# Kernel optimization log

Hardware: AMD Instinct MI355X
Metric: run time of the kernel (lower is better)

The kernel has to match this reference:

```python
import jax, jax.numpy as jnp
import numpy as np

TAU = 2.0       # LIF membrane time constant (spikingjelly default)
ALPHA = 2.0     # ATan surrogate sharpness
EPS = 1e-5      # BN eps
NUM_HEADS = 12
PATCH = 2
LENTH = 256     # (H/PATCH)*(W/PATCH)

@jax.custom_vjp
def heaviside(x):
    return (x >= 0.0).astype(x.dtype)

def _hv_fwd(x):
    return heaviside(x), x

def _hv_bwd(x, g):
    sg = ALPHA / 2.0 / (1.0 + (jnp.pi / 2.0 * ALPHA * x) ** 2)  # ATan surrogate
    return (g * sg,)

heaviside.defvjp(_hv_fwd, _hv_bwd)

def lif(x):
    # multi-step LIF over leading time axis, hard reset, v_th = 1.0
    def step(v, xt):
        v = v + (xt - v) / TAU
        s = heaviside(v - 1.0)
        return v * (1.0 - s), s
    _, s = jax.lax.scan(step, jnp.zeros_like(x[0]), x)
    return s

def setup_inputs() -> dict:
    key = jax.random.key(0)
    ks = jax.random.split(key, 9)
    T, B, C, H, W = 4, 4, 384, 32, 32
    x = jax.random.normal(ks[0], (T, B, C, H, W), dtype=jnp.float32)
    Wconv = jax.random.normal(ks[1], (2 * C, C, PATCH, PATCH), dtype=jnp.float32) * (1.0 / np.sqrt(C * PATCH * PATCH))
    gamma1 = jax.random.uniform(ks[2], (2 * C,), dtype=jnp.float32, minval=0.5, maxval=1.5)
    beta1 = jax.random.normal(ks[3], (2 * C,), dtype=jnp.float32) * 0.1
    Wproj = jax.random.normal(ks[4], (C, C), dtype=jnp.float32) * (1.0 / np.sqrt(C))
    gamma2 = jax.random.uniform(ks[5], (C,), dtype=jnp.float32, minval=0.5, maxval=1.5)
    beta2 = jax.random.normal(ks[6], (C,), dtype=jnp.float32) * 0.1
    firing_rate_x = jax.random.uniform(ks[7], (1, 1, NUM_HEADS, 1, 1), dtype=jnp.float32, minval=0.05, maxval=0.5)
    firing_rate_attn = jax.random.uniform(ks[8], (1, 1, NUM_HEADS, 1, 1), dtype=jnp.float32, minval=0.05, maxval=0.5)
    return {"x": x, "Wconv": Wconv, "gamma1": gamma1, "beta1": beta1, "Wproj": Wproj,
            "gamma2": gamma2, "beta2": beta2, "firing_rate_x": firing_rate_x,
            "firing_rate_attn": firing_rate_attn}

def reference(x, Wconv, gamma1, beta1, Wproj, gamma2, beta2, firing_rate_x, firing_rate_attn):
    T, B, C, H, W = x.shape
    d = C // NUM_HEADS
    xs = lif(x)                                          # spikes [T,B,C,H,W]
    # patch conv dim -> 2*dim, stride = kernel = PATCH (eval BN: running mean 0, var 1)
    y = jax.lax.conv_general_dilated(xs.reshape(T * B, C, H, W), Wconv,
                                     (PATCH, PATCH), 'VALID',
                                     dimension_numbers=('NCHW', 'OIHW', 'NCHW'))
    bn1 = gamma1 / jnp.sqrt(1.0 + EPS)
    y = y * bn1[None, :, None, None] + beta1[None, :, None, None]
    Np = (H // PATCH) * (W // PATCH)                     # == LENTH
    y = y.reshape(T, B, NUM_HEADS, 2 * d, Np)
    y1, y2 = y[:, :, :, :d, :], y[:, :, :, d:, :]
    xr = xs.reshape(T, B, NUM_HEADS, d, H * W)
    scale1 = 1.0 / jnp.sqrt(firing_rate_x * d)
    attn = jnp.einsum('tbhdn,tbhdm->tbhnm', y1, xr) * scale1   # [T,B,h,Np,HW]
    attn = lif(attn)
    scale2 = 1.0 / jnp.sqrt(firing_rate_attn * LENTH)
    out = jnp.einsum('tbhdn,tbhnm->tbhdm', y2, attn) * scale2  # [T,B,h,d,HW]
    out = out.reshape(T, B, C, H, W)
    out = lif(out)
    out = jnp.einsum('oc,tbchw->tbohw', Wproj, out)            # 1x1 conv proj
    bn2 = gamma2 / jnp.sqrt(1.0 + EPS)
    out = out * bn2[None, None, :, None, None] + beta2[None, None, :, None, None]
    return out + x
```

## Files before the change

kernel.cpp:

```cpp
#include <hip/hip_runtime.h>
#include <hip/hip_bf16.h>
#include <math.h>


typedef __attribute__((ext_vector_type(8))) short short8;
typedef __attribute__((ext_vector_type(4))) float f32x4;

#define T_ 4
#define B_ 4
#define C_ 384
#define HW 1024
#define NH_ 12
#define Np_ 256
#define EPS_ 1e-5f

static __device__ __forceinline__ unsigned short f2bf(float f) {
    __hip_bfloat16 h = __float2bfloat16(f);
    return *reinterpret_cast<unsigned short*>(&h);
}
static __device__ __forceinline__ float bf2f(unsigned short u) {
    __hip_bfloat16 h = *reinterpret_cast<__hip_bfloat16*>(&u);
    return __bfloat162float(h);
}
static __device__ __forceinline__ void split3(float w, unsigned short& u0,
                                              unsigned short& u1, unsigned short& u2) {
    u0 = f2bf(w);  float f0 = bf2f(u0);
    float r1 = w - f0;
    u1 = f2bf(r1); float f1 = bf2f(u1);
    u2 = f2bf(r1 - f1);
}

__global__ __launch_bounds__(256) void k_wsplit(const float* __restrict__ Wc,
                                                const float* __restrict__ Wp,
                                                unsigned short* __restrict__ Wc3,
                                                unsigned short* __restrict__ Wp3) {
    const int NC = 768 * 1536;
    const int NP = 384 * 384;
    int i = blockIdx.x * 256 + threadIdx.x;
    float w; unsigned short* dst; int idx, plane;
    if (i < NC) { w = Wc[i]; dst = Wc3; idx = i; plane = NC; }
    else {
        int j = i - NC;
        if (j >= NP) return;
        w = Wp[j]; dst = Wp3; idx = j; plane = NP;
    }
    unsigned short u0, u1, u2;
    split3(w, u0, u1, u2);
    dst[idx] = u0; dst[plane + idx] = u1; dst[2 * plane + idx] = u2;
}

__global__ __launch_bounds__(256) void k_lif_im2col(const float* __restrict__ x,
                                                    unsigned short* __restrict__ Bc,
                                                    unsigned short* __restrict__ xsb) {
    int gt = blockIdx.x * 256 + threadIdx.x;
    int pw = gt & 15, ph = (gt >> 4) & 15;
    int v = gt >> 8;
    int c = v % 384, b = v / 384;
    float v00 = 0.f, v01 = 0.f, v10 = 0.f, v11 = 0.f;
    const size_t xrow = ((size_t)b * C_ + c) * HW + (size_t)(2 * ph) * 32 + 2 * pw;
#pragma unroll
    for (int t = 0; t < T_; ++t) {
        const float* px = x + (size_t)t * (B_ * C_ * HW) + xrow;
        float2 r0 = *(const float2*)px;
        float2 r1 = *(const float2*)(px + 32);
        v00 += (r0.x - v00) * 0.5f;
        v01 += (r0.y - v01) * 0.5f;
        v10 += (r1.x - v10) * 0.5f;
        v11 += (r1.y - v11) * 0.5f;
        ushort4 s;
        s.x = (v00 >= 1.f) ? 0x3F80 : 0; if (v00 >= 1.f) v00 = 0.f;
        s.y = (v01 >= 1.f) ? 0x3F80 : 0; if (v01 >= 1.f) v01 = 0.f;
        s.z = (v10 >= 1.f) ? 0x3F80 : 0; if (v10 >= 1.f) v10 = 0.f;
        s.w = (v11 >= 1.f) ? 0x3F80 : 0; if (v11 >= 1.f) v11 = 0.f;
        int tb = t * B_ + b;
        int n = tb * 256 + ph * 16 + pw;
        *(ushort4*)(Bc + (size_t)n * 1536 + 4 * c) = s;
        size_t xo = ((size_t)tb * C_ + c) * HW + (size_t)(2 * ph) * 32 + 2 * pw;
        ushort2 w0 = {s.x, s.y}, w1 = {s.z, s.w};
        *(ushort2*)(xsb + xo) = w0;
        *(ushort2*)(xsb + xo + 32) = w1;
    }
}

#define GL16(GP, LP) __builtin_amdgcn_global_load_lds(                        \
    (const __attribute__((address_space(1))) void*)(GP),                      \
    (__attribute__((address_space(3))) void*)(LP), 16, 0, 0)

static __device__ __forceinline__ void stage_conv(const unsigned short* __restrict__ Wc3,
                                                  const unsigned short* __restrict__ Bc,
                                                  short* smb, int mb, int nb, int k0,
                                                  int wid, int rloc, int cswz) {
    if (wid == 0) {
#pragma unroll
        for (int s = 0; s < 3; ++s)
#pragma unroll
            for (int u = 0; u < 2; ++u)
                GL16(Wc3 + ((size_t)(s * 768 + mb * 32 + u * 16 + rloc)) * 1536 + k0 + cswz * 8,
                     smb + s * 1024 + u * 512);
        GL16(Bc + ((size_t)(nb * 128 + rloc)) * 1536 + k0 + cswz * 8, smb + 3072);
    } else {
#pragma unroll
        for (int v = 1; v < 8; ++v)
            GL16(Bc + ((size_t)(nb * 128 + v * 16 + rloc)) * 1536 + k0 + cswz * 8,
                 smb + 3072 + v * 512);
    }
}

__global__ __launch_bounds__(128) void k_mconv(const unsigned short* __restrict__ Bc,
                                               const unsigned short* __restrict__ Wc3,
                                               const float* __restrict__ g1,
                                               const float* __restrict__ b1,
                                               const float* __restrict__ frx,
                                               const float* __restrict__ fra,
                                               unsigned short* __restrict__ y1s,
                                               unsigned short* __restrict__ y2s) {
    __shared__ short sm[3][7168];
    const int nb = blockIdx.x, mb = blockIdx.y;
    const int tid = threadIdx.x;
    const int lane = tid & 63, wid = tid >> 6;
    const int quad = lane >> 4, lr = lane & 15;
    const int rloc = lane >> 2;
    const int cswz = (lane & 3) ^ ((lane >> 3) & 3);
    const int slot = quad ^ ((lr >> 1) & 3);
    const int wn = wid;

    f32x4 acc[2][4];
#pragma unroll
    for (int im = 0; im < 2; ++im)
#pragma unroll
        for (int in = 0; in < 4; ++in)
            acc[im][in] = (f32x4){0.f, 0.f, 0.f, 0.f};

    stage_conv(Wc3, Bc, sm[0], mb, nb, 0, wid, rloc, cswz);
    stage_conv(Wc3, Bc, sm[1], mb, nb, 32, wid, rloc, cswz);

#pragma unroll 3
    for (int kt = 0; kt < 48; ++kt) {
        if (kt < 47) { asm volatile("s_waitcnt vmcnt(7)" ::: "memory"); }
        else         { asm volatile("s_waitcnt vmcnt(0)" ::: "memory"); }
        asm volatile("" ::: "memory");
        __builtin_amdgcn_s_barrier();
        __builtin_amdgcn_sched_barrier(0);

        if (kt <= 45)
            stage_conv(Wc3, Bc, sm[(kt + 2) % 3], mb, nb, (kt + 2) * 32, wid, rloc, cswz);

        const short* smb = sm[kt % 3];
        short8 af[3][2], bf[4];
#pragma unroll
        for (int s = 0; s < 3; ++s)
#pragma unroll
            for (int im = 0; im < 2; ++im)
                af[s][im] = *(const short8*)&smb[s * 1024 + (im * 16 + lr) * 32 + slot * 8];
#pragma unroll
        for (int in = 0; in < 4; ++in)
            bf[in] = *(const short8*)&smb[3072 + (wn * 64 + in * 16 + lr) * 32 + slot * 8];

#pragma unroll
        for (int s = 0; s < 3; ++s)
#pragma unroll
            for (int im = 0; im < 2; ++im)
#pragma unroll
                for (int in = 0; in < 4; ++in)
                    acc[im][in] = __builtin_amdgcn_mfma_f32_16x16x32_bf16(af[s][im], bf[in], acc[im][in], 0, 0, 0);
    }

    const float rs = 1.0f / sqrtf(1.0f + EPS_);
    const int h = mb >> 1, half = mb & 1;
    const float scl = (half == 0) ? (1.0f / sqrtf(frx[h] * 32.0f))
                                  : (1.0f / sqrtf(fra[h] * 256.0f));
    unsigned short* dst = (half == 0) ? y1s : y2s;
#pragma unroll
    for (int im = 0; im < 2; ++im) {
#pragma unroll
        for (int in = 0; in < 4; ++in) {
            int n_g = nb * 128 + wn * 64 + in * 16 + lr;
            int tb = n_g >> 8, pn = n_g & 255;
            size_t base = (size_t)(tb * NH_ + h) * 3 * 8192;
            ushort4 o0, o1, o2;
#pragma unroll
            for (int r = 0; r < 4; ++r) {
                int oc = mb * 32 + im * 16 + quad * 4 + r;
                float val = (acc[im][in][r] * (g1[oc] * rs) + b1[oc]) * scl;
                unsigned short u0, u1, u2;
                split3(val, u0, u1, u2);
                ((unsigned short*)&o0)[r] = u0;
                ((unsigned short*)&o1)[r] = u1;
                ((unsigned short*)&o2)[r] = u2;
            }
            int dd = im * 16 + quad * 4;
            if (half == 0) {
                *(ushort4*)&dst[base + 0 * 8192 + (size_t)pn * 32 + dd] = o0;
                *(ushort4*)&dst[base + 1 * 8192 + (size_t)pn * 32 + dd] = o1;
                *(ushort4*)&dst[base + 2 * 8192 + (size_t)pn * 32 + dd] = o2;
            } else {
#pragma unroll
                for (int r = 0; r < 4; ++r) {
                    dst[base + 0 * 8192 + (size_t)(dd + r) * 256 + pn] = ((unsigned short*)&o0)[r];
                    dst[base + 1 * 8192 + (size_t)(dd + r) * 256 + pn] = ((unsigned short*)&o1)[r];
                    dst[base + 2 * 8192 + (size_t)(dd + r) * 256 + pn] = ((unsigned short*)&o2)[r];
                }
            }
        }
    }
}

__global__ __launch_bounds__(256, 2) void k_attn_qk(const unsigned short* __restrict__ xsb,
                                                    const unsigned short* __restrict__ y1s,
                                                    unsigned short* __restrict__ abq) {
    __shared__ unsigned short xb[4][64][40];
    const int h = blockIdx.y, b = blockIdx.z;
    const int tid = threadIdx.x;
    const int lane = tid & 63, wq = tid >> 6;
    const int quad = lane >> 4, lr = lane & 15;
    const int m0 = blockIdx.x * 64;

#pragma unroll
    for (int i = 0; i < 8; ++i) {
        int e = tid + i * 256;
        int j4 = e & 15, d = (e >> 4) & 31, t = e >> 9;
        ushort4 v = *(const ushort4*)(xsb + ((size_t)((t * B_ + b) * C_) + h * 32 + d) * HW + m0 + j4 * 4);
        int key = (j4 ^ (j4 >> 2)) & 3;
        int cc = ((((d >> 3) ^ key) << 3) | (d & 7));
        xb[t][j4 * 4 + 0][cc] = v.x;
        xb[t][j4 * 4 + 1][cc] = v.y;
        xb[t][j4 * 4 + 2][cc] = v.z;
        xb[t][j4 * 4 + 3][cc] = v.w;
    }
    __syncthreads();

    float vat[4][4][4];
#pragma unroll
    for (int mi = 0; mi < 4; ++mi)
#pragma unroll
        for (int itl = 0; itl < 4; ++itl)
#pragma unroll
            for (int r = 0; r < 4; ++r) vat[mi][itl][r] = 0.f;

#pragma unroll
    for (int t = 0; t < T_; ++t) {
        const int tb = t * B_ + b;
        const size_t slab = (size_t)(tb * NH_ + h) * 3 * 8192;

        short8 af[3][4];
        const unsigned short* y1p = y1s + slab + (size_t)(wq * 64 + lr) * 32 + quad * 8;
#pragma unroll
        for (int s = 0; s < 3; ++s)
#pragma unroll
            for (int itl = 0; itl < 4; ++itl)
                af[s][itl] = *(const short8*)(y1p + s * 8192 + itl * 512);

#pragma unroll
        for (int mi = 0; mi < 4; ++mi) {
            int keyr = ((lr >> 2) ^ mi) & 3;
            short8 bx = *(const short8*)&xb[t][mi * 16 + lr][(quad ^ keyr) * 8];
            f32x4 acc[4];
#pragma unroll
            for (int itl = 0; itl < 4; ++itl) acc[itl] = (f32x4){0.f, 0.f, 0.f, 0.f};
#pragma unroll
            for (int s = 0; s < 3; ++s)
#pragma unroll
                for (int itl = 0; itl < 4; ++itl)
                    acc[itl] = __builtin_amdgcn_mfma_f32_16x16x32_bf16(af[s][itl], bx, acc[itl], 0, 0, 0);

            unsigned int q = 0;
#pragma unroll
            for (int itl = 0; itl < 4; ++itl)
#pragma unroll
                for (int r = 0; r < 4; ++r) {
                    float v = vat[mi][itl][r];
                    v += (acc[itl][r] - v) * 0.5f;
                    bool s = (v >= 1.0f);
                    vat[mi][itl][r] = s ? 0.f : v;
                    q |= (s ? 1u : 0u) << (itl * 4 + r);
                }
            int m = m0 + mi * 16 + lr;
            abq[(((size_t)(tb * NH_ + h) * 1024 + m) * 4 + quad) * 4 + wq] = (unsigned short)q;
        }
    }
}

__global__ __launch_bounds__(128) void k_attn_pv(const unsigned long long* __restrict__ abits,
                                                 const unsigned short* __restrict__ y2s,
                                                 unsigned short* __restrict__ obt) {
    const int h = blockIdx.y, b = blockIdx.z;
    const int tid = threadIdx.x;
    const int lane = tid & 63;
    const int quad = lane >> 4, lr = lane & 15;
    const int dt = tid >> 6;
    const int mbase = blockIdx.x * 64;
    const int obase = (quad & 2) << 1;

    float vo[4][4];
#pragma unroll
    for (int mi = 0; mi < 4; ++mi)
#pragma unroll
        for (int r = 0; r < 4; ++r) vo[mi][r] = 0.f;

#pragma unroll
    for (int t = 0; t < T_; ++t) {
        const int tb = t * B_ + b;
        const size_t slab = (size_t)(tb * NH_ + h) * 3 * 8192;

        short8 ay[3][8];
        const unsigned short* y2p = y2s + slab + (size_t)(dt * 16 + lr) * 256 + quad * 8;
#pragma unroll
        for (int s = 0; s < 3; ++s)
#pragma unroll
            for (int kt = 0; kt < 8; ++kt)
                ay[s][kt] = *(const short8*)(y2p + s * 8192 + kt * 32);

#pragma unroll
        for (int mi = 0; mi < 4; ++mi) {
            const int m = mbase + mi * 16 + lr;
            const unsigned long long* ap = abits + ((size_t)(tb * NH_ + h) * 1024 + m) * 4 + (quad & 1) * 2;
            unsigned long long Qa = ap[0];
            unsigned long long Qb = ap[1];

            short8 bs[8];
#pragma unroll
            for (int kt = 0; kt < 8; ++kt) {
                int o = kt * 8 + obase;
                unsigned int a4 = (unsigned int)(Qa >> o) & 15u;
                unsigned int b4 = (unsigned int)(Qb >> o) & 15u;
                union { short8 v; unsigned int w[4]; } u;
                u.w[0] = ((a4 & 1u) ? 0x3F80u : 0u) | ((a4 & 2u) ? 0x3F800000u : 0u);
                u.w[1] = ((a4 & 4u) ? 0x3F80u : 0u) | ((a4 & 8u) ? 0x3F800000u : 0u);
                u.w[2] = ((b4 & 1u) ? 0x3F80u : 0u) | ((b4 & 2u) ? 0x3F800000u : 0u);
                u.w[3] = ((b4 & 4u) ? 0x3F80u : 0u) | ((b4 & 8u) ? 0x3F800000u : 0u);
                bs[kt] = u.v;
            }

            f32x4 acc2 = (f32x4){0.f, 0.f, 0.f, 0.f};
#pragma unroll
            for (int s = 0; s < 3; ++s)
#pragma unroll
                for (int kt = 0; kt < 8; ++kt)
                    acc2 = __builtin_amdgcn_mfma_f32_16x16x32_bf16(ay[s][kt], bs[kt], acc2, 0, 0, 0);

            ushort4 ob;
#pragma unroll
            for (int r = 0; r < 4; ++r) {
                float v = vo[mi][r];
                v += (acc2[r] - v) * 0.5f;
                bool s = (v >= 1.0f);
                ((unsigned short*)&ob)[r] = s ? 0x3F80 : 0;
                vo[mi][r] = s ? 0.f : v;
            }
            *(ushort4*)(obt + ((size_t)tb * HW + m) * C_ + h * 32 + dt * 16 + quad * 4) = ob;
        }
    }
}

static __device__ __forceinline__ void stage_proj(const unsigned short* __restrict__ Wp3,
                                                  const unsigned short* __restrict__ obt,
                                                  short* smb, int mb, int nb, int k0,
                                                  int wid, int rloc, int cswz) {
    if (wid < 3) {
#pragma unroll
        for (int u = 0; u < 4; ++u)
            GL16(Wp3 + ((size_t)(wid * 384 + mb * 64 + u * 16 + rloc)) * 384 + k0 + cswz * 8,
                 smb + wid * 2048 + u * 512);
        GL16(obt + ((size_t)(nb * 128 + wid * 16 + rloc)) * 384 + k0 + cswz * 8,
             smb + 6144 + wid * 512);
    } else {
#pragma unroll
        for (int v = 3; v < 8; ++v)
            GL16(obt + ((size_t)(nb * 128 + v * 16 + rloc)) * 384 + k0 + cswz * 8,
                 smb + 6144 + v * 512);
    }
}

__global__ __launch_bounds__(256) void k_mproj(const unsigned short* __restrict__ obt,
                                               const unsigned short* __restrict__ Wp3,
                                               const float* __restrict__ g2,
                                               const float* __restrict__ b2,
                                               const float* __restrict__ x,
                                               float* __restrict__ out) {
    __shared__ short sm[2][10240];
    const int nb = blockIdx.x, mb = blockIdx.y;
    const int tid = threadIdx.x;
    const int lane = tid & 63, wave = tid >> 6;
    const int wm = wave >> 1, wn = wave & 1;
    const int quad = lane >> 4, lr = lane & 15;
    const int rloc = lane >> 2;
    const int cswz = (lane & 3) ^ ((lane >> 3) & 3);
    const int slot = quad ^ ((lr >> 1) & 3);

    f32x4 acc[2][4];
#pragma unroll
    for (int im = 0; im < 2; ++im)
#pragma unroll
        for (int in = 0; in < 4; ++in)
            acc[im][in] = (f32x4){0.f, 0.f, 0.f, 0.f};

    stage_proj(Wp3, obt, sm[0], mb, nb, 0, wave, rloc, cswz);

    for (int kt = 0; kt < 12; ++kt) {
        const int b = kt & 1;
        if (kt < 11) {
            stage_proj(Wp3, obt, sm[b ^ 1], mb, nb, (kt + 1) * 32, wave, rloc, cswz);
            asm volatile("s_waitcnt vmcnt(5)" ::: "memory");
        } else {
            asm volatile("s_waitcnt vmcnt(0)" ::: "memory");
        }
        __builtin_amdgcn_s_barrier();
        __builtin_amdgcn_sched_barrier(0);

        const short* smb = sm[b];
        short8 af[3][2], bf[4];
#pragma unroll
        for (int s = 0; s < 3; ++s)
#pragma unroll
            for (int im = 0; im < 2; ++im)
                af[s][im] = *(const short8*)&smb[s * 2048 + (wm * 32 + im * 16 + lr) * 32 + slot * 8];
#pragma unroll
        for (int in = 0; in < 4; ++in)
            bf[in] = *(const short8*)&smb[6144 + (wn * 64 + in * 16 + lr) * 32 + slot * 8];
        asm volatile("s_waitcnt lgkmcnt(0)" ::: "memory");
        __builtin_amdgcn_sched_barrier(0);
        __builtin_amdgcn_s_barrier();
        __builtin_amdgcn_sched_barrier(0);

#pragma unroll
        for (int s = 0; s < 3; ++s)
#pragma unroll
            for (int im = 0; im < 2; ++im)
#pragma unroll
                for (int in = 0; in < 4; ++in)
                    acc[im][in] = __builtin_amdgcn_mfma_f32_16x16x32_bf16(af[s][im], bf[in], acc[im][in], 0, 0, 0);
    }

    const float rs = 1.0f / sqrtf(1.0f + EPS_);
#pragma unroll
    for (int im = 0; im < 2; ++im) {
#pragma unroll
        for (int in = 0; in < 4; ++in) {
            int n_g = nb * 128 + wn * 64 + in * 16 + lr;
            int tb = n_g >> 10, hw = n_g & 1023;
#pragma unroll
            for (int r = 0; r < 4; ++r) {
                int o = mb * 64 + wm * 32 + im * 16 + quad * 4 + r;
                size_t idx = ((size_t)tb * C_ + o) * HW + hw;
                out[idx] = acc[im][in][r] * (g2[o] * rs) + b2[o] + x[idx];
            }
        }
    }
}

extern "C" void kernel_launch(void* const* d_in, const int* in_sizes, int n_in,
                              void* d_out, int out_size, void* d_ws, size_t ws_size,
                              hipStream_t stream) {
    const float* x      = (const float*)d_in[0];
    const float* Wconv  = (const float*)d_in[1];
    const float* gamma1 = (const float*)d_in[2];
    const float* beta1  = (const float*)d_in[3];
    const float* Wproj  = (const float*)d_in[4];
    const float* gamma2 = (const float*)d_in[5];
    const float* beta2  = (const float*)d_in[6];
    const float* frx    = (const float*)d_in[7];
    const float* fra    = (const float*)d_in[8];
    float* out = (float*)d_out;

    unsigned short* ws16 = (unsigned short*)d_ws;
    unsigned short* Bc  = ws16;
    unsigned short* obt = ws16;
    unsigned short* Wc3 = ws16 + 6291456;
    unsigned short* Wp3 = ws16 + 9830400;
    unsigned short* xsb = ws16 + 10272768;
    unsigned short* y1s = ws16 + 16564224;
    unsigned short* y2s = ws16 + 21282816;
    unsigned long long* abits = (unsigned long long*)(ws16 + 26001408);

    k_wsplit<<<5184, 256, 0, stream>>>(Wconv, Wproj, Wc3, Wp3);
    k_lif_im2col<<<1536, 256, 0, stream>>>(x, Bc, xsb);
    k_mconv<<<dim3(32, 24), 128, 0, stream>>>(Bc, Wc3, gamma1, beta1, frx, fra, y1s, y2s);
    k_attn_qk<<<dim3(16, 12, 4), 256, 0, stream>>>(xsb, y1s, (unsigned short*)abits);
    k_attn_pv<<<dim3(16, 12, 4), 128, 0, stream>>>(abits, y2s, obt);
    k_mproj<<<dim3(128, 6), 256, 0, stream>>>(obt, Wp3, gamma2, beta2, x, out);
}
```

Baseline: 243.8 us.

## Fuse QK and PV attention kernels via shared-memory spike bits; merge prep kernels

Merges the weight-split and LIF/im2col kernels into a single launch that dispatches on block index. Fuses the QK-spike and PV kernels so the attention spike bitmasks for each timestep are passed through a double-buffered shared-memory tile instead of a global round-trip. The work is redistributed across 4 waves (d-tile by m-group), and y2 fragments are loaded per split slice to lower register pressure. The gains come from fewer launches and no global attention-bit traffic. In exchange, the fused kernel adds a block barrier per timestep, drops the 2-blocks occupancy hint, and no longer unrolls the time loop.

```diff
diff --git a/kernel.cpp b/kernel.cpp
--- a/kernel.cpp
+++ b/kernel.cpp
@@ -30,55 +30,56 @@
     u2 = f2bf(r1 - f1);
 }
 
-__global__ __launch_bounds__(256) void k_wsplit(const float* __restrict__ Wc,
-                                                const float* __restrict__ Wp,
-                                                unsigned short* __restrict__ Wc3,
-                                                unsigned short* __restrict__ Wp3) {
-    const int NC = 768 * 1536;
-    const int NP = 384 * 384;
-    int i = blockIdx.x * 256 + threadIdx.x;
-    float w; unsigned short* dst; int idx, plane;
-    if (i < NC) { w = Wc[i]; dst = Wc3; idx = i; plane = NC; }
-    else {
-        int j = i - NC;
-        if (j >= NP) return;
-        w = Wp[j]; dst = Wp3; idx = j; plane = NP;
-    }
-    unsigned short u0, u1, u2;
-    split3(w, u0, u1, u2);
-    dst[idx] = u0; dst[plane + idx] = u1; dst[2 * plane + idx] = u2;
-}
-
-__global__ __launch_bounds__(256) void k_lif_im2col(const float* __restrict__ x,
-                                                    unsigned short* __restrict__ Bc,
-                                                    unsigned short* __restrict__ xsb) {
-    int gt = blockIdx.x * 256 + threadIdx.x;
-    int pw = gt & 15, ph = (gt >> 4) & 15;
-    int v = gt >> 8;
-    int c = v % 384, b = v / 384;
-    float v00 = 0.f, v01 = 0.f, v10 = 0.f, v11 = 0.f;
-    const size_t xrow = ((size_t)b * C_ + c) * HW + (size_t)(2 * ph) * 32 + 2 * pw;
-#pragma unroll
-    for (int t = 0; t < T_; ++t) {
-        const float* px = x + (size_t)t * (B_ * C_ * HW) + xrow;
-        float2 r0 = *(const float2*)px;
-        float2 r1 = *(const float2*)(px + 32);
-        v00 += (r0.x - v00) * 0.5f;
-        v01 += (r0.y - v01) * 0.5f;
-        v10 += (r1.x - v10) * 0.5f;
-        v11 += (r1.y - v11) * 0.5f;
-        ushort4 s;
-        s.x = (v00 >= 1.f) ? 0x3F80 : 0; if (v00 >= 1.f) v00 = 0.f;
-        s.y = (v01 >= 1.f) ? 0x3F80 : 0; if (v01 >= 1.f) v01 = 0.f;
-        s.z = (v10 >= 1.f) ? 0x3F80 : 0; if (v10 >= 1.f) v10 = 0.f;
-        s.w = (v11 >= 1.f) ? 0x3F80 : 0; if (v11 >= 1.f) v11 = 0.f;
-        int tb = t * B_ + b;
-        int n = tb * 256 + ph * 16 + pw;
-        *(ushort4*)(Bc + (size_t)n * 1536 + 4 * c) = s;
-        size_t xo = ((size_t)tb * C_ + c) * HW + (size_t)(2 * ph) * 32 + 2 * pw;
-        ushort2 w0 = {s.x, s.y}, w1 = {s.z, s.w};
-        *(ushort2*)(xsb + xo) = w0;
-        *(ushort2*)(xsb + xo + 32) = w1;
+__global__ __launch_bounds__(256) void k_pre(const float* __restrict__ Wc,
+                                             const float* __restrict__ Wp,
+                                             const float* __restrict__ x,
+                                             unsigned short* __restrict__ Wc3,
+                                             unsigned short* __restrict__ Wp3,
+                                             unsigned short* __restrict__ Bc,
+                                             unsigned short* __restrict__ xsb) {
+    if (blockIdx.x < 5184) {
+        const int NC = 768 * 1536;
+        const int NP = 384 * 384;
+        int i = blockIdx.x * 256 + threadIdx.x;
+        float w; unsigned short* dst; int idx, plane;
+        if (i < NC) { w = Wc[i]; dst = Wc3; idx = i; plane = NC; }
+        else {
+            int j = i - NC;
+            if (j >= NP) return;
+            w = Wp[j]; dst = Wp3; idx = j; plane = NP;
+        }
+        unsigned short u0, u1, u2;
+        split3(w, u0, u1, u2);
+        dst[idx] = u0; dst[plane + idx] = u1; dst[2 * plane + idx] = u2;
+    } else {
+        int gt = (blockIdx.x - 5184) * 256 + threadIdx.x;
+        int pw = gt & 15, ph = (gt >> 4) & 15;
+        int v = gt >> 8;
+        int c = v % 384, b = v / 384;
+        float v00 = 0.f, v01 = 0.f, v10 = 0.f, v11 = 0.f;
+        const size_t xrow = ((size_t)b * C_ + c) * HW + (size_t)(2 * ph) * 32 + 2 * pw;
+#pragma unroll
+        for (int t = 0; t < T_; ++t) {
+            const float* px = x + (size_t)t * (B_ * C_ * HW) + xrow;
+            float2 r0 = *(const float2*)px;
+            float2 r1 = *(const float2*)(px + 32);
+            v00 += (r0.x - v00) * 0.5f;
+            v01 += (r0.y - v01) * 0.5f;
+            v10 += (r1.x - v10) * 0.5f;
+            v11 += (r1.y - v11) * 0.5f;
+            ushort4 s;
+            s.x = (v00 >= 1.f) ? 0x3F80 : 0; if (v00 >= 1.f) v00 = 0.f;
+            s.y = (v01 >= 1.f) ? 0x3F80 : 0; if (v01 >= 1.f) v01 = 0.f;
+            s.z = (v10 >= 1.f) ? 0x3F80 : 0; if (v10 >= 1.f) v10 = 0.f;
+            s.w = (v11 >= 1.f) ? 0x3F80 : 0; if (v11 >= 1.f) v11 = 0.f;
+            int tb = t * B_ + b;
+            int n = tb * 256 + ph * 16 + pw;
+            *(ushort4*)(Bc + (size_t)n * 1536 + 4 * c) = s;
+            size_t xo = ((size_t)tb * C_ + c) * HW + (size_t)(2 * ph) * 32 + 2 * pw;
+            ushort2 w0 = {s.x, s.y}, w1 = {s.z, s.w};
+            *(ushort2*)(xsb + xo) = w0;
+            *(ushort2*)(xsb + xo + 32) = w1;
+        }
     }
 }
 
@@ -205,15 +206,20 @@
     }
 }
 
-__global__ __launch_bounds__(256, 2) void k_attn_qk(const unsigned short* __restrict__ xsb,
-                                                    const unsigned short* __restrict__ y1s,
-                                                    unsigned short* __restrict__ abq) {
+__global__ __launch_bounds__(256) void k_attn(const unsigned short* __restrict__ xsb,
+                                              const unsigned short* __restrict__ y1s,
+                                              const unsigned short* __restrict__ y2s,
+                                              unsigned short* __restrict__ obt) {
     __shared__ unsigned short xb[4][64][40];
+    __shared__ unsigned long long ab[2][64][4];
     const int h = blockIdx.y, b = blockIdx.z;
     const int tid = threadIdx.x;
-    const int lane = tid & 63, wq = tid >> 6;
+    const int lane = tid & 63, wv = tid >> 6;
     const int quad = lane >> 4, lr = lane & 15;
     const int m0 = blockIdx.x * 64;
+    const int wq = wv;
+    const int dt = wv >> 1, mg = wv & 1;
+    const int obase = (quad & 2) << 1;
 
 #pragma unroll
     for (int i = 0; i < 8; ++i) {
@@ -236,8 +242,12 @@
         for (int itl = 0; itl < 4; ++itl)
 #pragma unroll
             for (int r = 0; r < 4; ++r) vat[mi][itl][r] = 0.f;
-
-#pragma unroll
+    float vo[2][4];
+#pragma unroll
+    for (int mi = 0; mi < 2; ++mi)
+#pragma unroll
+        for (int r = 0; r < 4; ++r) vo[mi][r] = 0.f;
+
     for (int t = 0; t < T_; ++t) {
         const int tb = t * B_ + b;
         const size_t slab = (size_t)(tb * NH_ + h) * 3 * 8192;
@@ -274,48 +284,16 @@
                     vat[mi][itl][r] = s ? 0.f : v;
                     q |= (s ? 1u : 0u) << (itl * 4 + r);
                 }
-            int m = m0 + mi * 16 + lr;
-            abq[(((size_t)(tb * NH_ + h) * 1024 + m) * 4 + quad) * 4 + wq] = (unsigned short)q;
-        }
-    }
-}
-
-__global__ __launch_bounds__(128) void k_attn_pv(const unsigned long long* __restrict__ abits,
-                                                 const unsigned short* __restrict__ y2s,
-                                                 unsigned short* __restrict__ obt) {
-    const int h = blockIdx.y, b = blockIdx.z;
-    const int tid = threadIdx.x;
-    const int lane = tid & 63;
-    const int quad = lane >> 4, lr = lane & 15;
-    const int dt = tid >> 6;
-    const int mbase = blockIdx.x * 64;
-    const int obase = (quad & 2) << 1;
-
-    float vo[4][4];
-#pragma unroll
-    for (int mi = 0; mi < 4; ++mi)
-#pragma unroll
-        for (int r = 0; r < 4; ++r) vo[mi][r] = 0.f;
-
-#pragma unroll
-    for (int t = 0; t < T_; ++t) {
-        const int tb = t * B_ + b;
-        const size_t slab = (size_t)(tb * NH_ + h) * 3 * 8192;
-
-        short8 ay[3][8];
+            ((unsigned short*)&ab[t & 1][mi * 16 + lr][quad])[wq] = (unsigned short)q;
+        }
+        __syncthreads();
+
         const unsigned short* y2p = y2s + slab + (size_t)(dt * 16 + lr) * 256 + quad * 8;
 #pragma unroll
-        for (int s = 0; s < 3; ++s)
-#pragma unroll
-            for (int kt = 0; kt < 8; ++kt)
-                ay[s][kt] = *(const short8*)(y2p + s * 8192 + kt * 32);
-
-#pragma unroll
-        for (int mi = 0; mi < 4; ++mi) {
-            const int m = mbase + mi * 16 + lr;
-            const unsigned long long* ap = abits + ((size_t)(tb * NH_ + h) * 1024 + m) * 4 + (quad & 1) * 2;
-            unsigned long long Qa = ap[0];
-            unsigned long long Qb = ap[1];
+        for (int mi = 0; mi < 2; ++mi) {
+            const int mloc = mg * 32 + mi * 16 + lr;
+            unsigned long long Qa = ab[t & 1][mloc][(quad & 1) * 2];
+            unsigned long long Qb = ab[t & 1][mloc][(quad & 1) * 2 + 1];
 
             short8 bs[8];
 #pragma unroll
@@ -333,10 +311,15 @@
 
             f32x4 acc2 = (f32x4){0.f, 0.f, 0.f, 0.f};
 #pragma unroll
-            for (int s = 0; s < 3; ++s)
+            for (int s = 0; s < 3; ++s) {
+                short8 ays[8];
 #pragma unroll
                 for (int kt = 0; kt < 8; ++kt)
-                    acc2 = __builtin_amdgcn_mfma_f32_16x16x32_bf16(ay[s][kt], bs[kt], acc2, 0, 0, 0);
+                    ays[kt] = *(const short8*)(y2p + s * 8192 + kt * 32);
+#pragma unroll
+                for (int kt = 0; kt < 8; ++kt)
+                    acc2 = __builtin_amdgcn_mfma_f32_16x16x32_bf16(ays[kt], bs[kt], acc2, 0, 0, 0);
+            }
 
             ushort4 ob;
 #pragma unroll
@@ -347,6 +330,7 @@
                 ((unsigned short*)&ob)[r] = s ? 0x3F80 : 0;
                 vo[mi][r] = s ? 0.f : v;
             }
+            const int m = m0 + mloc;
             *(ushort4*)(obt + ((size_t)tb * HW + m) * C_ + h * 32 + dt * 16 + quad * 4) = ob;
         }
     }
@@ -470,12 +454,9 @@
     unsigned short* xsb = ws16 + 10272768;
     unsigned short* y1s = ws16 + 16564224;
     unsigned short* y2s = ws16 + 21282816;
-    unsigned long long* abits = (unsigned long long*)(ws16 + 26001408);
-
-    k_wsplit<<<5184, 256, 0, stream>>>(Wconv, Wproj, Wc3, Wp3);
-    k_lif_im2col<<<1536, 256, 0, stream>>>(x, Bc, xsb);
+
+    k_pre<<<6720, 256, 0, stream>>>(Wconv, Wproj, x, Wc3, Wp3, Bc, xsb);
     k_mconv<<<dim3(32, 24), 128, 0, stream>>>(Bc, Wc3, gamma1, beta1, frx, fra, y1s, y2s);
-    k_attn_qk<<<dim3(16, 12, 4), 256, 0, stream>>>(xsb, y1s, (unsigned short*)abits);
-    k_attn_pv<<<dim3(16, 12, 4), 128, 0, stream>>>(abits, y2s, obt);
+    k_attn<<<dim3(16, 12, 4), 256, 0, stream>>>(xsb, y1s, y2s, obt);
     k_mproj<<<dim3(128, 6), 256, 0, stream>>>(obt, Wp3, gamma2, beta2, x, out);
 }
```

After: 279.8 us. +14.8%, slower.
